# Performance work log

Hardware: AMD Instinct MI355X
Metric: run time of the kernel (lower is better)

Reference implementation:

```python
import jax, jax.numpy as jnp
import numpy as np

B, TQ, TK = 2, 2048, 2048
D, H, G = 1024, 16, 4
HD = D // H  # 64
MAX_LEN = 4096


def _rope(x, max_len):
    # x: [B, H, S, hd]; interleaved even/odd RoPE, freqs use full head_dim in denom
    hd = x.shape[-1]
    seq = x.shape[2]
    pos = jnp.arange(max_len, dtype=jnp.float32)[:, None]           # [max_len, 1]
    div = jnp.exp(jnp.arange(0, hd, 2, dtype=jnp.float32) * (-np.log(10000.0) / hd))
    sin = jnp.sin(pos * div)[:seq]                                   # [S, hd/2]
    cos = jnp.cos(pos * div)[:seq]
    xe, xo = x[..., 0::2], x[..., 1::2]
    oe = xe * cos - xo * sin
    oo = xe * sin + xo * cos
    return jnp.stack([oe, oo], axis=-1).reshape(x.shape)


def setup_inputs() -> dict:
    key = jax.random.key(0)
    ks = jax.random.split(key, 10)
    s = 0.02
    return {
        "X": jax.random.normal(ks[0], (B, TQ, D), jnp.float32),
        "encoder_output": jax.random.normal(ks[1], (B, TK, D), jnp.float32),
        "Wq": jax.random.normal(ks[2], (D, D), jnp.float32) * s,
        "bq": jnp.zeros((D,), jnp.float32),
        "Wk": jax.random.normal(ks[3], (D, G * HD), jnp.float32) * s,
        "bk": jnp.zeros((G * HD,), jnp.float32),
        "Wv": jax.random.normal(ks[4], (D, G * HD), jnp.float32) * s,
        "bv": jnp.zeros((G * HD,), jnp.float32),
        "Wo": jax.random.normal(ks[5], (D, D), jnp.float32) * s,
        "bo": jnp.zeros((D,), jnp.float32),
        "max_len": MAX_LEN,
    }


def reference(X, encoder_output, Wq, bq, Wk, bk, Wv, bv, Wo, bo, max_len):
    bsz, tq, d = X.shape
    q = X @ Wq + bq                       # [B, TQ, D]
    k = encoder_output @ Wk + bk          # [B, TK, G*HD]
    v = encoder_output @ Wv + bv

    q = q.reshape(bsz, tq, H, HD).transpose(0, 2, 1, 3)          # [B, H, TQ, HD]
    k = k.reshape(bsz, -1, G, HD).transpose(0, 2, 1, 3)          # [B, G, TK, HD]
    v = v.reshape(bsz, -1, G, HD).transpose(0, 2, 1, 3)
    # expand each group to H//G consecutive heads (matches torch expand+reshape)
    k = jnp.repeat(k, H // G, axis=1)                            # [B, H, TK, HD]
    v = jnp.repeat(v, H // G, axis=1)

    q = _rope(q, max_len)
    k = _rope(k, max_len)

    scores = jnp.einsum("bhqd,bhkd->bhqk", q, k) / jnp.sqrt(jnp.float32(HD))
    w = jax.nn.softmax(scores, axis=-1)
    o = jnp.einsum("bhqk,bhkd->bhqd", w, v)                      # [B, H, TQ, HD]
    o = o.transpose(0, 2, 1, 3).reshape(bsz, tq, d)
    return o @ Wo + bo
```

## Files before the change

kernel.cpp:

```cpp
#include <hip/hip_runtime.h>
#include <cstdint>


typedef __bf16 bf16x8 __attribute__((ext_vector_type(8)));
typedef __bf16 bf16x4v __attribute__((ext_vector_type(4)));
typedef float f32x4 __attribute__((ext_vector_type(4)));

#define MFMA16(a, b, c) __builtin_amdgcn_mfma_f32_16x16x32_bf16((a), (b), (c), 0, 0, 0)

constexpr int Bc = 2, TQc = 2048, TKc = 2048, Dc = 1024, Hc = 16, Gc = 4, HDc = 64;
constexpr float QSCALE = 0.18033688011112042f;

__device__ __forceinline__ ushort bfbits(float x) {
  __bf16 h = (__bf16)x;
  return __builtin_bit_cast(ushort, h);
}

__device__ __forceinline__ float fexp2(float x) {
  float r;
  asm("v_exp_f32 %0, %1" : "=v"(r) : "v"(x));
  return r;
}

__device__ __forceinline__ float fmax3(float a, float b, float c) {
  return fmaxf(fmaxf(a, b), c);
}

__device__ __forceinline__ void async_lds16(void* lds, const void* g) {
  __builtin_amdgcn_global_load_lds((const __attribute__((address_space(1))) uint32_t*)g,
                                   (__attribute__((address_space(3))) uint32_t*)lds,
                                   16, 0, 0);
}

__global__ __launch_bounds__(256) void prep_k(const float* __restrict__ X,
                                              const float* __restrict__ E,
                                              const float* __restrict__ Wq,
                                              const float* __restrict__ Wo,
                                              const float* __restrict__ Wk,
                                              const float* __restrict__ Wv,
                                              ushort* __restrict__ Xb,
                                              ushort* __restrict__ Eb,
                                              ushort* __restrict__ Wqt,
                                              ushort* __restrict__ Wot,
                                              ushort* __restrict__ Wkvt) {
  __shared__ float t[64][65];
  const int bid = blockIdx.x;
  if (bid < 8192) {
    const float* s = (bid < 4096) ? X : E;
    ushort* d = (bid < 4096) ? Xb : Eb;
    int i = (bid & 4095) * 256 + threadIdx.x;
    float4 v = reinterpret_cast<const float4*>(s)[i];
    ushort4 o;
    o.x = bfbits(v.x); o.y = bfbits(v.y); o.z = bfbits(v.z); o.w = bfbits(v.w);
    reinterpret_cast<ushort4*>(d)[i] = o;
    return;
  }
  const int w = bid - 8192;
  const int z = w >> 8, rem = w & 255;
  const int bx = rem & 15, by = rem >> 4;
  const float* src;
  ushort* dst;
  int C, c0;
  if (z == 0)      { src = Wq; dst = Wqt; C = 1024; c0 = bx * 64; }
  else if (z == 1) { src = Wo; dst = Wot; C = 1024; c0 = bx * 64; }
  else {
    if (bx >= 8) return;
    if (bx < 4) { src = Wk; dst = Wkvt; }
    else        { src = Wv; dst = Wkvt + 256 * 1024; }
    C = 256; c0 = (bx & 3) * 64;
  }
  const int r0 = by * 64;
  const int tx = threadIdx.x & 63, ty = threadIdx.x >> 6;
#pragma unroll
  for (int i = 0; i < 16; ++i) {
    int r = i * 4 + ty;
    t[r][tx] = src[(size_t)(r0 + r) * C + c0 + tx];
  }
  __syncthreads();
#pragma unroll
  for (int i = 0; i < 16; ++i) {
    int c = i * 4 + ty;
    dst[(size_t)(c0 + c) * 1024 + r0 + tx] = bfbits(t[tx][c]);
  }
}

__device__ __forceinline__ void gemm_mainloop(const ushort* __restrict__ A,
                                              const ushort* __restrict__ Bt,
                                              int m0, int n0, int K,
                                              char* sA, char* sB,
                                              f32x4 acc[4][2]) {
  const int lane = threadIdx.x & 63, wid = threadIdx.x >> 6;
  const int l15 = lane & 15, l4 = lane >> 4;
  const int wr = (wid >> 1) * 64, wc = (wid & 1) * 32;
  const int srow = lane >> 3;
  const int scc = (lane & 7) ^ (srow & 7);
  const int rxr = l15 & 7;

  const int nsteps = K >> 6;
#pragma unroll
  for (int j = 0; j < 4; ++j) {
    int c = wid * 4 + j;
    async_lds16(sA + c * 1024, A + (size_t)(m0 + c * 8 + srow) * K + scc * 8);
  }
#pragma unroll
  for (int j = 0; j < 2; ++j) {
    int c = wid * 2 + j;
    async_lds16(sB + c * 1024, Bt + (size_t)(n0 + c * 8 + srow) * K + scc * 8);
  }
  __syncthreads();

  int buf = 0;
  for (int s2 = 0; s2 < nsteps; ++s2) {
    if (s2 + 1 < nsteps) {
      const int k0 = (s2 + 1) * 64;
      char* dA = sA + (buf ^ 1) * 16384;
      char* dB = sB + (buf ^ 1) * 8192;
#pragma unroll
      for (int j = 0; j < 4; ++j) {
        int c = wid * 4 + j;
        async_lds16(dA + c * 1024, A + (size_t)(m0 + c * 8 + srow) * K + k0 + scc * 8);
      }
#pragma unroll
      for (int j = 0; j < 2; ++j) {
        int c = wid * 2 + j;
        async_lds16(dB + c * 1024, Bt + (size_t)(n0 + c * 8 + srow) * K + k0 + scc * 8);
      }
    }
    const char* aB = sA + buf * 16384;
    const char* bB = sB + buf * 8192;
    bf16x8 af[2][4], bfr[2][2];
#pragma unroll
    for (int mi = 0; mi < 4; ++mi) {
      const int row = wr + mi * 16 + l15;
#pragma unroll
      for (int kk = 0; kk < 2; ++kk)
        af[kk][mi] = *reinterpret_cast<const bf16x8*>(
            aB + row * 128 + (((l4 + kk * 4) ^ rxr) << 4));
    }
#pragma unroll
    for (int ni = 0; ni < 2; ++ni) {
      const int row = wc + ni * 16 + l15;
#pragma unroll
      for (int kk = 0; kk < 2; ++kk)
        bfr[kk][ni] = *reinterpret_cast<const bf16x8*>(
            bB + row * 128 + (((l4 + kk * 4) ^ rxr) << 4));
    }
#pragma unroll
    for (int kk = 0; kk < 2; ++kk)
#pragma unroll
      for (int mi = 0; mi < 4; ++mi)
#pragma unroll
        for (int ni = 0; ni < 2; ++ni)
          acc[mi][ni] = MFMA16(af[kk][mi], bfr[kk][ni], acc[mi][ni]);
    __syncthreads();
    buf ^= 1;
  }
}

__device__ __forceinline__ void gemm_epilogue(f32x4 acc[4][2], int mode, int m0,
                                              int n0, const float* b0,
                                              const float* b1, float* Cf,
                                              ushort* U0, ushort* U1, int N) {
  const int lane = threadIdx.x & 63, wid = threadIdx.x >> 6;
  const int l15 = lane & 15, l4 = lane >> 4;
  const int wr = (wid >> 1) * 64, wc = (wid & 1) * 32;
#pragma unroll
  for (int ni = 0; ni < 2; ++ni) {
    const int col = n0 + wc + ni * 16 + l15;
    if (mode == 0) {
      const float bv = b0[col];
#pragma unroll
      for (int mi = 0; mi < 4; ++mi) {
        const int rowb = m0 + wr + mi * 16 + l4 * 4;
#pragma unroll
        for (int r = 0; r < 4; ++r)
          Cf[(size_t)(rowb + r) * N + col] = acc[mi][ni][r] + bv;
      }
    } else if (mode == 1) {
      const int h = col >> 6, d = col & 63, fi = d >> 1, odd = d & 1;
      const float div = __expf(-0.28782313662425572f * (float)fi);
      const float bv = b0[col];
#pragma unroll
      for (int mi = 0; mi < 4; ++mi) {
        const int rowb = m0 + wr + mi * 16 + l4 * 4;
#pragma unroll
        for (int r = 0; r < 4; ++r) {
          const int row = rowb + r, b = row >> 11, t = row & 2047;
          const float val = acc[mi][ni][r] + bv;
          const float prt = __shfl_xor(val, 1);
          float sn, cs;
          __sincosf((float)t * div, &sn, &cs);
          const float o = odd ? (prt * sn + val * cs) : (val * cs - prt * sn);
          U0[(((size_t)(b * Hc + h)) * TQc + t) * HDc + d] = bfbits(o * QSCALE);
        }
      }
    } else {
      if (col < 256) {
        const int g = col >> 6, d = col & 63, fi = d >> 1, odd = d & 1;
        const float div = __expf(-0.28782313662425572f * (float)fi);
        const float bv = b0[col];
#pragma unroll
        for (int mi = 0; mi < 4; ++mi) {
          const int rowb = m0 + wr + mi * 16 + l4 * 4;
#pragma unroll
          for (int r = 0; r < 4; ++r) {
            const int row = rowb + r, b = row >> 11, t = row & 2047;
            const float val = acc[mi][ni][r] + bv;
            const float prt = __shfl_xor(val, 1);
            float sn, cs;
            __sincosf((float)t * div, &sn, &cs);
            const float o = odd ? (prt * sn + val * cs) : (val * cs - prt * sn);
            U0[(((size_t)(b * Gc + g)) * TKc + t) * HDc + d] = bfbits(o);
          }
        }
      } else {
        const int c2 = col - 256;
        const int g = c2 >> 6, d = c2 & 63;
        const float bv = b1[c2];
#pragma unroll
        for (int mi = 0; mi < 4; ++mi) {
          const int rowb = m0 + wr + mi * 16 + l4 * 4;
          const int b = rowb >> 11, t0 = rowb & 2047;
          ushort4 w;
          w.x = bfbits(acc[mi][ni][0] + bv);
          w.y = bfbits(acc[mi][ni][1] + bv);
          w.z = bfbits(acc[mi][ni][2] + bv);
          w.w = bfbits(acc[mi][ni][3] + bv);
          *reinterpret_cast<ushort4*>(
              &U1[(((size_t)(b * Gc + g)) * HDc + d) * TKc + t0]) = w;
        }
      }
    }
  }
}

__global__ __launch_bounds__(256) void qkv_k(const ushort* __restrict__ Xb,
                                             const ushort* __restrict__ Eb,
                                             const ushort* __restrict__ Wqt,
                                             const ushort* __restrict__ Wkvt,
                                             const float* __restrict__ bq,
                                             const float* __restrict__ bk,
                                             const float* __restrict__ bv,
                                             ushort* __restrict__ Qb,
                                             ushort* __restrict__ Kb,
                                             ushort* __restrict__ Vt) {
  __shared__ __attribute__((aligned(16))) char smem[48 * 1024];
  const int bid = blockIdx.x;
  const ushort *A, *Bt;
  const float *b0, *b1 = nullptr;
  ushort *U0, *U1 = nullptr;
  int mode, tb, tn;
  if (bid < 512) { A = Xb; Bt = Wqt; b0 = bq; U0 = Qb; mode = 1; tb = bid; tn = 16; }
  else { A = Eb; Bt = Wkvt; b0 = bk; b1 = bv; U0 = Kb; U1 = Vt; mode = 2; tb = bid - 512; tn = 8; }
  const int m0 = (tb / tn) * 128, n0 = (tb % tn) * 64;
  const f32x4 z = {0.f, 0.f, 0.f, 0.f};
  f32x4 acc[4][2] = {{z, z}, {z, z}, {z, z}, {z, z}};
  gemm_mainloop(A, Bt, m0, n0, 1024, smem, smem + 32768, acc);
  gemm_epilogue(acc, mode, m0, n0, b0, b1, nullptr, U0, U1, 0);
}

__global__ __launch_bounds__(256) void oproj_k(const ushort* __restrict__ Ob,
                                               const ushort* __restrict__ Wot,
                                               const float* __restrict__ bo,
                                               float* __restrict__ out) {
  __shared__ __attribute__((aligned(16))) char smem[48 * 1024];
  const int bid = blockIdx.x;
  const int m0 = (bid >> 4) * 128, n0 = (bid & 15) * 64;
  const f32x4 z = {0.f, 0.f, 0.f, 0.f};
  f32x4 acc[4][2] = {{z, z}, {z, z}, {z, z}, {z, z}};
  gemm_mainloop(Ob, Wot, m0, n0, 1024, smem, smem + 32768, acc);
  gemm_epilogue(acc, 0, m0, n0, bo, nullptr, out, nullptr, nullptr, 1024);
}

__global__ __launch_bounds__(1024, 4) void attn_k(const ushort* __restrict__ Qg,
                                                  const ushort* __restrict__ Kg,
                                                  const ushort* __restrict__ Vg,
                                                  ushort* __restrict__ Ob) {
  __shared__ __attribute__((aligned(16))) char smem[64 * 1024];
  const int lane = threadIdx.x & 63, wid = threadIdx.x >> 6;
  const int l15 = lane & 15, l4 = lane >> 4;
  const int bid = blockIdx.x;
  const int bg = bid & 7, pos = bid >> 3;
  const int b = bg >> 2, g = bg & 3;
  const int h = g * 4 + (pos >> 3);
  const int q0 = (pos & 7) * 256 + wid * 16;
  const ushort* Qp = Qg + ((size_t)(b * Hc + h)) * TQc * HDc;
  const ushort* Kp = Kg + ((size_t)(b * Gc + g)) * TKc * HDc;
  const ushort* Vp = Vg + ((size_t)(b * Gc + g)) * HDc * TKc;
  char* sK = smem;
  char* sV = smem + 16384;
  char* pb = smem + 32768 + wid * 2048;
  const int rx = (l15 & 7) << 4;
  const int swz = l15 & 7;

  const int wkv = wid & 7;
  const int sr = wkv * 8 + (lane >> 3);
  const int sc = (lane & 7) ^ ((lane >> 3) & 7);
  const bool isK = (wid < 8);
  const char* srcN = isK ? (const char*)Kp + (size_t)sr * 128 + sc * 16
                         : (const char*)Vp + (size_t)sr * (TKc * 2) + sc * 16;
  const size_t srcStep = isK ? 8192 : 128;
  char* dstBase = (isK ? sK : sV) + wkv * 1024;

  bf16x8 bq0 = *reinterpret_cast<const bf16x8*>(Qp + (size_t)(q0 + l15) * HDc + l4 * 8);
  bf16x8 bq1 = *reinterpret_cast<const bf16x8*>(Qp + (size_t)(q0 + l15) * HDc + 32 + l4 * 8);

  bf16x8 vones;
#pragma unroll
  for (int i = 0; i < 8; ++i) vones[i] = (__bf16)1.0f;

  float m = -INFINITY;
  const f32x4 z = {0.f, 0.f, 0.f, 0.f};
  f32x4 accO[4] = {z, z, z, z};
  f32x4 acc1 = z;

  constexpr int NT = TKc / 64;
  async_lds16(dstBase, srcN);
  srcN += srcStep;
  __syncthreads();

  int buf = 0;
  for (int kt = 0; kt < NT; ++kt) {
    if (kt + 1 < NT) {
      async_lds16(dstBase + (buf ^ 1) * 8192, srcN);
      srcN += srcStep;
    }
    const char* sKb = sK + buf * 8192;
    const char* sVb = sV + buf * 8192;

    f32x4 s[4] = {z, z, z, z};
#pragma unroll
    for (int nf = 0; nf < 4; ++nf) {
      const char* krow = sKb + (nf * 16 + l15) * 128;
      bf16x8 kf0 = *reinterpret_cast<const bf16x8*>(krow + ((l4 ^ swz) << 4));
      bf16x8 kf1 = *reinterpret_cast<const bf16x8*>(krow + (((4 + l4) ^ swz) << 4));
      s[nf] = MFMA16(kf0, bq0, s[nf]);
      s[nf] = MFMA16(kf1, bq1, s[nf]);
    }
    bf16x8 va[4][2];
#pragma unroll
    for (int df = 0; df < 4; ++df) {
      const char* vrow = sVb + (df * 16 + l15) * 128;
      va[df][0] = *reinterpret_cast<const bf16x8*>(vrow + ((l4 ^ swz) << 4));
      va[df][1] = *reinterpret_cast<const bf16x8*>(vrow + (((4 + l4) ^ swz) << 4));
    }

    float pm = fmax3(fmax3(s[0][0], s[0][1], s[0][2]),
                     fmax3(s[0][3], s[1][0], s[1][1]),
                     fmax3(s[1][2], s[1][3], s[2][0]));
    pm = fmax3(pm,
               fmax3(s[2][1], s[2][2], s[2][3]),
               fmax3(s[3][0], s[3][1], fmaxf(s[3][2], s[3][3])));
    pm = fmaxf(pm, __shfl_xor(pm, 16));
    pm = fmaxf(pm, __shfl_xor(pm, 32));
    if (!__all(pm - m <= 11.5f)) {
      float mn = fmaxf(m, pm);
      float sc2 = fexp2(m - mn);
      m = mn;
      acc1 *= sc2;
#pragma unroll
      for (int df = 0; df < 4; ++df) accO[df] *= sc2;
    }
#pragma unroll
    for (int nf = 0; nf < 4; ++nf)
#pragma unroll
      for (int r = 0; r < 4; ++r)
        s[nf][r] = fexp2(s[nf][r] - m);

#pragma unroll
    for (int nf = 0; nf < 4; ++nf) {
      bf16x4v pv;
      pv[0] = (__bf16)s[nf][0];
      pv[1] = (__bf16)s[nf][1];
      pv[2] = (__bf16)s[nf][2];
      pv[3] = (__bf16)s[nf][3];
      *reinterpret_cast<uint2*>(pb + l15 * 128 + ((nf * 32 + l4 * 8) ^ rx)) =
          __builtin_bit_cast(uint2, pv);
    }
    asm volatile("" ::: "memory");
    bf16x8 ap0 = *reinterpret_cast<const bf16x8*>(pb + l15 * 128 + ((l4 * 16) ^ rx));
    bf16x8 ap1 = *reinterpret_cast<const bf16x8*>(pb + l15 * 128 + ((64 + l4 * 16) ^ rx));
#pragma unroll
    for (int df = 0; df < 4; ++df)
      accO[df] = MFMA16(ap1, va[df][1], MFMA16(ap0, va[df][0], accO[df]));
    acc1 = MFMA16(ap1, vones, MFMA16(ap0, vones, acc1));

    __syncthreads();
    buf ^= 1;
  }

  float inv[4];
#pragma unroll
  for (int r = 0; r < 4; ++r) inv[r] = 1.f / acc1[r];
#pragma unroll
  for (int df = 0; df < 4; ++df)
#pragma unroll
    for (int r = 0; r < 4; ++r) {
      int row = q0 + l4 * 4 + r;
      int col = h * HDc + df * 16 + l15;
      Ob[((size_t)b * TQc + row) * Dc + col] = bfbits(accO[df][r] * inv[r]);
    }
}

extern "C" void kernel_launch(void* const* d_in, const int* in_sizes, int n_in,
                              void* d_out, int out_size, void* d_ws, size_t ws_size,
                              hipStream_t stream) {
  const float* X  = (const float*)d_in[0];
  const float* E  = (const float*)d_in[1];
  const float* Wq = (const float*)d_in[2];
  const float* bq = (const float*)d_in[3];
  const float* Wk = (const float*)d_in[4];
  const float* bk = (const float*)d_in[5];
  const float* Wv = (const float*)d_in[6];
  const float* bv = (const float*)d_in[7];
  const float* Wo = (const float*)d_in[8];
  const float* bo = (const float*)d_in[9];
  float* out = (float*)d_out;
  char* ws = (char*)d_ws;

  const size_t MB = 1ull << 20;
  if (ws_size < 42 * MB) return;

  ushort* Xb   = (ushort*)(ws + 0 * MB);
  ushort* Eb   = (ushort*)(ws + 8 * MB);
  ushort* Wqt  = (ushort*)(ws + 16 * MB);
  ushort* Wkvt = (ushort*)(ws + 18 * MB);
  ushort* Wot  = (ushort*)(ws + 19 * MB);
  ushort* Qb   = (ushort*)(ws + 21 * MB);
  ushort* Kb   = (ushort*)(ws + 29 * MB);
  ushort* Vt   = (ushort*)(ws + 31 * MB);
  ushort* Ob   = (ushort*)(ws + 33 * MB);

  prep_k<<<dim3(8960), 256, 0, stream>>>(X, E, Wq, Wo, Wk, Wv, Xb, Eb, Wqt, Wot, Wkvt);
  qkv_k<<<dim3(768), 256, 0, stream>>>(Xb, Eb, Wqt, Wkvt, bq, bk, bv, Qb, Kb, Vt);
  attn_k<<<dim3(256), dim3(1024), 0, stream>>>(Qb, Kb, Vt, Ob);
  oproj_k<<<dim3(512), 256, 0, stream>>>(Ob, Wot, bo, out);
}
```

Before: 100.2 us.

## Use 128x128 GEMM tiles with K=32 stages and a new LDS swizzle

The projection GEMM mainloop now uses 128x128 output tiles (4x4 MFMA accumulators per wave) in place of 128x64, with 32-wide K steps. It uses a new paired-row LDS layout and swizzle, which cuts LDS to 32 KB. The grid sizes for the QKV and output-projection kernels are halved to match. This raises arithmetic intensity per loaded byte, at the cost of fewer blocks (384 and 256 on a large-CU part), more register pressure, and twice as many K-loop iterations with a barrier each.

```diff
diff --git a/kernel.cpp b/kernel.cpp
--- a/kernel.cpp
+++ b/kernel.cpp
@@ -87,85 +87,71 @@
 __device__ __forceinline__ void gemm_mainloop(const ushort* __restrict__ A,
                                               const ushort* __restrict__ Bt,
                                               int m0, int n0, int K,
-                                              char* sA, char* sB,
-                                              f32x4 acc[4][2]) {
+                                              char* smem, f32x4 acc[4][4]) {
   const int lane = threadIdx.x & 63, wid = threadIdx.x >> 6;
   const int l15 = lane & 15, l4 = lane >> 4;
-  const int wr = (wid >> 1) * 64, wc = (wid & 1) * 32;
-  const int srow = lane >> 3;
-  const int scc = (lane & 7) ^ (srow & 7);
-  const int rxr = l15 & 7;
-
-  const int nsteps = K >> 6;
-#pragma unroll
-  for (int j = 0; j < 4; ++j) {
-    int c = wid * 4 + j;
-    async_lds16(sA + c * 1024, A + (size_t)(m0 + c * 8 + srow) * K + scc * 8);
-  }
-#pragma unroll
-  for (int j = 0; j < 2; ++j) {
-    int c = wid * 2 + j;
-    async_lds16(sB + c * 1024, Bt + (size_t)(n0 + c * 8 + srow) * K + scc * 8);
-  }
+  const int wr = (wid >> 1) * 64, wc = (wid & 1) * 64;
+  const int sp8 = lane >> 3;
+  const int scl = (lane & 7) ^ sp8;
+  const int slr = 2 * sp8 + (scl >> 2);
+  const int sko = (scl & 3) * 8;
+
+  char* bufA[2] = {smem, smem + 8192};
+  char* bufB[2] = {smem + 16384, smem + 24576};
+
+  const int nsteps = K >> 5;
+  auto stage = [&](int step, int bi) {
+    const int k0 = step * 32;
+#pragma unroll
+    for (int j = 0; j < 2; ++j) {
+      const int i = wid * 2 + j;
+      const int lr = i * 16 + slr;
+      async_lds16(bufA[bi] + i * 1024, A + (size_t)(m0 + lr) * K + k0 + sko);
+      async_lds16(bufB[bi] + i * 1024, Bt + (size_t)(n0 + lr) * K + k0 + sko);
+    }
+  };
+
+  stage(0, 0);
   __syncthreads();
-
   int buf = 0;
   for (int s2 = 0; s2 < nsteps; ++s2) {
-    if (s2 + 1 < nsteps) {
-      const int k0 = (s2 + 1) * 64;
-      char* dA = sA + (buf ^ 1) * 16384;
-      char* dB = sB + (buf ^ 1) * 8192;
-#pragma unroll
-      for (int j = 0; j < 4; ++j) {
-        int c = wid * 4 + j;
-        async_lds16(dA + c * 1024, A + (size_t)(m0 + c * 8 + srow) * K + k0 + scc * 8);
-      }
-#pragma unroll
-      for (int j = 0; j < 2; ++j) {
-        int c = wid * 2 + j;
-        async_lds16(dB + c * 1024, Bt + (size_t)(n0 + c * 8 + srow) * K + k0 + scc * 8);
-      }
-    }
-    const char* aB = sA + buf * 16384;
-    const char* bB = sB + buf * 8192;
-    bf16x8 af[2][4], bfr[2][2];
+    if (s2 + 1 < nsteps) stage(s2 + 1, buf ^ 1);
+    const char* aB = bufA[buf];
+    const char* bB = bufB[buf];
+    bf16x8 af[4], bfr[4];
 #pragma unroll
     for (int mi = 0; mi < 4; ++mi) {
-      const int row = wr + mi * 16 + l15;
-#pragma unroll
-      for (int kk = 0; kk < 2; ++kk)
-        af[kk][mi] = *reinterpret_cast<const bf16x8*>(
-            aB + row * 128 + (((l4 + kk * 4) ^ rxr) << 4));
-    }
-#pragma unroll
-    for (int ni = 0; ni < 2; ++ni) {
-      const int row = wc + ni * 16 + l15;
-#pragma unroll
-      for (int kk = 0; kk < 2; ++kk)
-        bfr[kk][ni] = *reinterpret_cast<const bf16x8*>(
-            bB + row * 128 + (((l4 + kk * 4) ^ rxr) << 4));
-    }
-#pragma unroll
-    for (int kk = 0; kk < 2; ++kk)
-#pragma unroll
-      for (int mi = 0; mi < 4; ++mi)
-#pragma unroll
-        for (int ni = 0; ni < 2; ++ni)
-          acc[mi][ni] = MFMA16(af[kk][mi], bfr[kk][ni], acc[mi][ni]);
+      const int R = wr + mi * 16 + l15;
+      const int p = R >> 1;
+      const int sl = (((R & 1) << 2) | l4) ^ (p & 7);
+      af[mi] = *reinterpret_cast<const bf16x8*>(aB + p * 128 + (sl << 4));
+    }
+#pragma unroll
+    for (int ni = 0; ni < 4; ++ni) {
+      const int R = wc + ni * 16 + l15;
+      const int p = R >> 1;
+      const int sl = (((R & 1) << 2) | l4) ^ (p & 7);
+      bfr[ni] = *reinterpret_cast<const bf16x8*>(bB + p * 128 + (sl << 4));
+    }
+#pragma unroll
+    for (int mi = 0; mi < 4; ++mi)
+#pragma unroll
+      for (int ni = 0; ni < 4; ++ni)
+        acc[mi][ni] = MFMA16(af[mi], bfr[ni], acc[mi][ni]);
     __syncthreads();
     buf ^= 1;
   }
 }
 
-__device__ __forceinline__ void gemm_epilogue(f32x4 acc[4][2], int mode, int m0,
+__device__ __forceinline__ void gemm_epilogue(f32x4 acc[4][4], int mode, int m0,
                                               int n0, const float* b0,
                                               const float* b1, float* Cf,
                                               ushort* U0, ushort* U1, int N) {
   const int lane = threadIdx.x & 63, wid = threadIdx.x >> 6;
   const int l15 = lane & 15, l4 = lane >> 4;
-  const int wr = (wid >> 1) * 64, wc = (wid & 1) * 32;
-#pragma unroll
-  for (int ni = 0; ni < 2; ++ni) {
+  const int wr = (wid >> 1) * 64, wc = (wid & 1) * 64;
+#pragma unroll
+  for (int ni = 0; ni < 4; ++ni) {
     const int col = n0 + wc + ni * 16 + l15;
     if (mode == 0) {
       const float bv = b0[col];
@@ -244,18 +230,22 @@
                                              ushort* __restrict__ Qb,
                                              ushort* __restrict__ Kb,
                                              ushort* __restrict__ Vt) {
-  __shared__ __attribute__((aligned(16))) char smem[48 * 1024];
+  __shared__ __attribute__((aligned(16))) char smem[32 * 1024];
   const int bid = blockIdx.x;
   const ushort *A, *Bt;
   const float *b0, *b1 = nullptr;
   ushort *U0, *U1 = nullptr;
   int mode, tb, tn;
-  if (bid < 512) { A = Xb; Bt = Wqt; b0 = bq; U0 = Qb; mode = 1; tb = bid; tn = 16; }
-  else { A = Eb; Bt = Wkvt; b0 = bk; b1 = bv; U0 = Kb; U1 = Vt; mode = 2; tb = bid - 512; tn = 8; }
-  const int m0 = (tb / tn) * 128, n0 = (tb % tn) * 64;
+  if (bid < 256) { A = Xb; Bt = Wqt; b0 = bq; U0 = Qb; mode = 1; tb = bid; tn = 8; }
+  else { A = Eb; Bt = Wkvt; b0 = bk; b1 = bv; U0 = Kb; U1 = Vt; mode = 2; tb = bid - 256; tn = 4; }
+  const int m0 = (tb / tn) * 128, n0 = (tb % tn) * 128;
   const f32x4 z = {0.f, 0.f, 0.f, 0.f};
-  f32x4 acc[4][2] = {{z, z}, {z, z}, {z, z}, {z, z}};
-  gemm_mainloop(A, Bt, m0, n0, 1024, smem, smem + 32768, acc);
+  f32x4 acc[4][4];
+#pragma unroll
+  for (int mi = 0; mi < 4; ++mi)
+#pragma unroll
+    for (int ni = 0; ni < 4; ++ni) acc[mi][ni] = z;
+  gemm_mainloop(A, Bt, m0, n0, 1024, smem, acc);
   gemm_epilogue(acc, mode, m0, n0, b0, b1, nullptr, U0, U1, 0);
 }
 
@@ -263,12 +253,16 @@
                                                const ushort* __restrict__ Wot,
                                                const float* __restrict__ bo,
                                                float* __restrict__ out) {
-  __shared__ __attribute__((aligned(16))) char smem[48 * 1024];
+  __shared__ __attribute__((aligned(16))) char smem[32 * 1024];
   const int bid = blockIdx.x;
-  const int m0 = (bid >> 4) * 128, n0 = (bid & 15) * 64;
+  const int m0 = (bid >> 3) * 128, n0 = (bid & 7) * 128;
   const f32x4 z = {0.f, 0.f, 0.f, 0.f};
-  f32x4 acc[4][2] = {{z, z}, {z, z}, {z, z}, {z, z}};
-  gemm_mainloop(Ob, Wot, m0, n0, 1024, smem, smem + 32768, acc);
+  f32x4 acc[4][4];
+#pragma unroll
+  for (int mi = 0; mi < 4; ++mi)
+#pragma unroll
+    for (int ni = 0; ni < 4; ++ni) acc[mi][ni] = z;
+  gemm_mainloop(Ob, Wot, m0, n0, 1024, smem, acc);
   gemm_epilogue(acc, 0, m0, n0, bo, nullptr, out, nullptr, nullptr, 1024);
 }
 
@@ -432,7 +426,7 @@
   ushort* Ob   = (ushort*)(ws + 33 * MB);
 
   prep_k<<<dim3(8960), 256, 0, stream>>>(X, E, Wq, Wo, Wk, Wv, Xb, Eb, Wqt, Wot, Wkvt);
-  qkv_k<<<dim3(768), 256, 0, stream>>>(Xb, Eb, Wqt, Wkvt, bq, bk, bv, Qb, Kb, Vt);
+  qkv_k<<<dim3(384), 256, 0, stream>>>(Xb, Eb, Wqt, Wkvt, bq, bk, bv, Qb, Kb, Vt);
   attn_k<<<dim3(256), dim3(1024), 0, stream>>>(Qb, Kb, Vt, Ob);
-  oproj_k<<<dim3(512), 256, 0, stream>>>(Ob, Wot, bo, out);
-}
+  oproj_k<<<dim3(256), 256, 0, stream>>>(Ob, Wot, bo, out);
+}
```

Result: slower. 127.0 us (+26.7%).
